# Performance work log

Hardware: AMD Instinct MI355X
Metric: run time of the kernel (lower is better)

The kernel has to match this reference:

```python
import jax, jax.numpy as jnp
import numpy as np

IN_CH = 2
K = 5
STRIDE = 1
NQ = IN_CH * K          # n_qubits = kernel_size * in_channels
DIM = 2 ** NQ           # quantum state dimension = 1024


def setup_inputs() -> dict:
    key = jax.random.key(0)
    k1, k2, k3 = jax.random.split(key, 3)
    x = jax.random.normal(k1, (16, IN_CH, 4096), dtype=jnp.float32)
    entangle_matrix = jax.random.normal(k2, (DIM, DIM), dtype=jnp.float32) / np.sqrt(DIM).astype(np.float32)
    theta = jax.random.uniform(k3, (NQ,), dtype=jnp.float32, minval=0.0, maxval=2.0 * np.pi)
    return {"x": x, "entangle_matrix": entangle_matrix, "theta": theta}


def _im2col(x):
    # torch: unfold(-1,K,stride) -> (B,C,nW,K); cat over channel dim along -1 -> (B,nW,C*K)
    B, C, L = x.shape
    nW = (L - K) // STRIDE + 1
    idx = jnp.arange(nW)[:, None] * STRIDE + jnp.arange(K)[None, :]   # (nW, K)
    cols = x[:, :, idx]                                               # (B, C, nW, K)
    cols = jnp.transpose(cols, (0, 2, 1, 3)).reshape(B * nW, C * K)   # channel-major last dim
    return cols, nW


def reference(x, entangle_matrix, theta):
    cols, nW = _im2col(x)           # (N, NQ) rotation angles, one per qubit
    N = cols.shape[0]
    # --- RY(x_i) angle encoding from |0...0>: product state of [cos(x/2), sin(x/2)] ---
    half = 0.5 * cols
    c, s = jnp.cos(half), jnp.sin(half)          # (N, NQ)
    state = jnp.ones((N, 1), dtype=x.dtype)
    for i in range(NQ):                          # loop over fixed small n_qubits
        qi = jnp.stack([c[:, i], s[:, i]], axis=-1)            # (N, 2)
        state = (state[:, :, None] * qi[:, None, :]).reshape(N, -1)
    # --- entangling layer: psi' = E @ psi (the custom kernel matmul) ---
    state = state @ entangle_matrix.T            # (N, DIM)
    # --- trainable per-qubit RY(theta_i) layer ---
    ct, st = jnp.cos(0.5 * theta), jnp.sin(0.5 * theta)
    for i in range(NQ):
        s4 = state.reshape(N, 2 ** i, 2, 2 ** (NQ - 1 - i))
        a0, a1 = s4[:, :, 0], s4[:, :, 1]
        state = jnp.stack([ct[i] * a0 - st[i] * a1,
                           st[i] * a0 + ct[i] * a1], axis=2).reshape(N, DIM)
    # --- measure <Z> on qubit 0 (most significant bit) ---
    p = (state * state).reshape(N, 2, DIM // 2)
    z = p[:, 0].sum(-1) - p[:, 1].sum(-1)        # (N,)
    B = x.shape[0]
    return z.reshape(B, 1, -1, nW)
```

## Files before the change

kernel.cpp:

```cpp
#include <hip/hip_runtime.h>
#include <math.h>

#define B_SZ   16
#define L_SZ   4096
#define NWIN   4092
#define U3     243
#define UPAD   256

#define APK_OFF 0
#define M_OFF   65536
#define EXTRA_OFF (M_OFF + 1048576)

typedef __attribute__((ext_vector_type(8))) __bf16 bf16x8;
typedef __attribute__((ext_vector_type(4))) float f32x4;

__device__ __forceinline__ float sel3(int t, float c, float s) {
    return t == 0 ? 1.0f : (t == 1 ? c : s);
}

__device__ __forceinline__ int apk_idx(int u, int v) {
    return (((u >> 4) * 8 + (v >> 5)) * 64 + ((u & 15) | (((v >> 3) & 3) << 4))) * 8 + (v & 7);
}

__device__ __forceinline__ void bfsplit(float x, float& hf, float& lf) {
    hf = __uint_as_float(__float_as_uint(x) & 0xFFFF0000u);
    lf = x - hf;
}

__global__ __launch_bounds__(256, 4) void mgemm_ker(const float* __restrict__ E,
                                                    const float* __restrict__ theta,
                                                    float* __restrict__ M,
                                                    float* __restrict__ Mp_extra) {
    __shared__ float SA[32][72];
    __shared__ float SB[32][72];
    __shared__ uint4 AfH[4 * 64], AfL[4 * 64];
    __shared__ uint4 BfH[4 * 64], BfL[4 * 64];

    int t = blockIdx.x;
    int bj = 0;
    while (t >= 16 - bj) { t -= 16 - bj; ++bj; }
    int bk = bj + t;
    int ks = blockIdx.z;
    int tid = threadIdx.x;
    int lane = tid & 63;
    int wave = tid >> 6;

    float th = theta[0];
    float st, ct;
    __sincosf(th, &st, &ct);

    f32x4 acc[4];
    #pragma unroll
    for (int kt = 0; kt < 4; ++kt) acc[kt] = (f32x4){0.f, 0.f, 0.f, 0.f};

    int kchunk = 1024 / gridDim.z;
    int k0 = ks * kchunk;
    int lr = tid >> 3;
    int lcq = (tid & 7) * 8;

    for (int d0 = k0; d0 < k0 + kchunk; d0 += 32) {
        bool hi = d0 >= 512;
        int dp = hi ? (d0 - 512) : (d0 + 512);
        float4 a0 = *(const float4*)&E[(d0 + lr) * 1024 + bj * 64 + lcq];
        float4 a1 = *(const float4*)&E[(d0 + lr) * 1024 + bj * 64 + lcq + 4];
        float4 q0 = *(const float4*)&E[(d0 + lr) * 1024 + bk * 64 + lcq];
        float4 q1 = *(const float4*)&E[(d0 + lr) * 1024 + bk * 64 + lcq + 4];
        float4 p0 = *(const float4*)&E[(dp + lr) * 1024 + bk * 64 + lcq];
        float4 p1 = *(const float4*)&E[(dp + lr) * 1024 + bk * 64 + lcq + 4];
        float4 y0, y1;
        if (!hi) {
            y0.x = ct * q0.x - st * p0.x; y0.y = ct * q0.y - st * p0.y;
            y0.z = ct * q0.z - st * p0.z; y0.w = ct * q0.w - st * p0.w;
            y1.x = ct * q1.x - st * p1.x; y1.y = ct * q1.y - st * p1.y;
            y1.z = ct * q1.z - st * p1.z; y1.w = ct * q1.w - st * p1.w;
        } else {
            y0.x = -st * p0.x - ct * q0.x; y0.y = -st * p0.y - ct * q0.y;
            y0.z = -st * p0.z - ct * q0.z; y0.w = -st * p0.w - ct * q0.w;
            y1.x = -st * p1.x - ct * q1.x; y1.y = -st * p1.y - ct * q1.y;
            y1.z = -st * p1.z - ct * q1.z; y1.w = -st * p1.w - ct * q1.w;
        }
        __syncthreads();
        *(float4*)&SA[lr][lcq] = a0;
        *(float4*)&SA[lr][lcq + 4] = a1;
        *(float4*)&SB[lr][lcq] = y0;
        *(float4*)&SB[lr][lcq + 4] = y1;
        __syncthreads();

        {
            unsigned ahw[4], alw[4], bhw[4], blw[4];
            float pah, pal, pbh, pbl;
            #pragma unroll
            for (int i = 0; i < 8; ++i) {
                float av = SA[wave * 8 + i][lane];
                float bv = SB[wave * 8 + i][lane];
                float ah, al, bh, bl;
                bfsplit(av, ah, al);
                bfsplit(bv, bh, bl);
                if (i & 1) {
                    ahw[i >> 1] = __byte_perm(__float_as_uint(pah), __float_as_uint(ah), 0x7632);
                    alw[i >> 1] = __byte_perm(__float_as_uint(pal), __float_as_uint(al), 0x7632);
                    bhw[i >> 1] = __byte_perm(__float_as_uint(pbh), __float_as_uint(bh), 0x7632);
                    blw[i >> 1] = __byte_perm(__float_as_uint(pbl), __float_as_uint(bl), 0x7632);
                } else { pah = ah; pal = al; pbh = bh; pbl = bl; }
            }
            int slot = ((lane >> 4) << 6) + (lane & 15) + (wave << 4);
            AfH[slot] = make_uint4(ahw[0], ahw[1], ahw[2], ahw[3]);
            AfL[slot] = make_uint4(alw[0], alw[1], alw[2], alw[3]);
            BfH[slot] = make_uint4(bhw[0], bhw[1], bhw[2], bhw[3]);
            BfL[slot] = make_uint4(blw[0], blw[1], blw[2], blw[3]);
        }
        __syncthreads();

        uint4 ahu = AfH[wave * 64 + lane];
        uint4 alu = AfL[wave * 64 + lane];
        bf16x8 ah = __builtin_bit_cast(bf16x8, ahu);
        bf16x8 al = __builtin_bit_cast(bf16x8, alu);
        #pragma unroll
        for (int kt = 0; kt < 4; ++kt) {
            uint4 bhu = BfH[kt * 64 + lane];
            uint4 blu = BfL[kt * 64 + lane];
            bf16x8 bh = __builtin_bit_cast(bf16x8, bhu);
            bf16x8 bl = __builtin_bit_cast(bf16x8, blu);
            acc[kt] = __builtin_amdgcn_mfma_f32_16x16x32_bf16(ah, bh, acc[kt], 0, 0, 0);
            acc[kt] = __builtin_amdgcn_mfma_f32_16x16x32_bf16(ah, bl, acc[kt], 0, 0, 0);
            acc[kt] = __builtin_amdgcn_mfma_f32_16x16x32_bf16(al, bh, acc[kt], 0, 0, 0);
        }
    }

    float* dst = (ks == 0) ? M : (Mp_extra + (ks - 1) * 1048576);
    #pragma unroll
    for (int kt = 0; kt < 4; ++kt) {
        #pragma unroll
        for (int i = 0; i < 4; ++i) {
            int r = bj * 64 + wave * 16 + ((lane >> 4) << 2) + i;
            int c = bk * 64 + kt * 16 + (lane & 15);
            dst[((r >> 5) * 32 + (c >> 5)) * 1024 + (r & 31) * 32 + (c & 31)] = acc[kt][i];
        }
    }
}

__global__ __launch_bounds__(256) void sum_ker(float* __restrict__ M,
                                               const float* __restrict__ Mp_extra,
                                               int S) {
    int i = blockIdx.x * 256 + threadIdx.x;
    float4 v = ((const float4*)M)[i];
    for (int s = 1; s < S; ++s) {
        float4 p = ((const float4*)(Mp_extra + (s - 1) * 1048576))[i];
        v.x += p.x; v.y += p.y; v.z += p.z; v.w += p.w;
    }
    ((float4*)M)[i] = v;
}

__global__ __launch_bounds__(256) void cwht_ker(const float* __restrict__ M,
                                                unsigned short* __restrict__ ApkH) {
    __shared__ float D[1024];
    int mx = blockIdx.x;
    int mxh = mx >> 5, mxl = mx & 31;
    int tid = threadIdx.x;
    float v[4];
    #pragma unroll
    for (int k = 0; k < 4; ++k) {
        int j = tid + k * 256;
        int jh = j >> 5, jl = j & 31;
        int kh = jh ^ mxh, kl = jl ^ mxl;
        int off;
        if ((jh >> 1) <= (kh >> 1)) off = ((jh * 32 + kh) * 32 + jl) * 32 + kl;
        else                        off = ((kh * 32 + jh) * 32 + kl) * 32 + jl;
        v[k] = M[off];
    }
    #pragma unroll
    for (int s = 0; s < 6; ++s) {
        int bit = (tid >> s) & 1;
        #pragma unroll
        for (int k = 0; k < 4; ++k) {
            float p = __shfl_xor(v[k], 1 << s, 64);
            v[k] = bit ? (p - v[k]) : (v[k] + p);
        }
    }
    #pragma unroll
    for (int k = 0; k < 4; ++k) D[tid + k * 256] = v[k];
    __syncthreads();
    {
        int b6 = (tid >> 6) & 1, b7 = (tid >> 7) & 1;
        #pragma unroll
        for (int k = 0; k < 4; ++k) {
            float p64  = D[(tid ^ 64)  + k * 256];
            float p128 = D[(tid ^ 128) + k * 256];
            float p192 = D[(tid ^ 192) + k * 256];
            float ta = b6 ? (p64 - v[k])   : (v[k] + p64);
            float tb = b6 ? (p192 - p128)  : (p128 + p192);
            v[k] = b7 ? (tb - ta) : (ta + tb);
        }
    }
    {
        float a0 = v[0] + v[1], a1 = v[0] - v[1], a2 = v[2] + v[3], a3 = v[2] - v[3];
        v[0] = a0 + a2; v[1] = a1 + a3; v[2] = a0 - a2; v[3] = a1 - a3;
    }
    #pragma unroll
    for (int k = 0; k < 4; ++k) {
        int mz = tid + k * 256;
        if (mz & mx) continue;
        int u = 0, vv = 0;
        #pragma unroll
        for (int i = 0; i < 5; ++i) {
            int bit = 9 - i;
            int tt = ((mx >> bit) & 1) ? 2 : (((mz >> bit) & 1) ? 1 : 0);
            u = u * 3 + tt;
        }
        #pragma unroll
        for (int i = 5; i < 10; ++i) {
            int bit = 9 - i;
            int tt = ((mx >> bit) & 1) ? 2 : (((mz >> bit) & 1) ? 1 : 0);
            vv = vv * 3 + tt;
        }
        float val = v[k] * (1.0f / 1024.0f);
        unsigned hh = __float_as_uint(val) & 0xFFFF0000u;
        float lf = val - __uint_as_float(hh);
        unsigned ll = __float_as_uint(lf) >> 16;
        int idx = apk_idx(u, vv);
        ApkH[idx] = (unsigned short)(hh >> 16);
        ApkH[idx + 65536] = (unsigned short)ll;
    }
    if (mx == 0) {
        for (int e = tid; e < 13 * 256; e += 256) {
            int u = 243 + (e >> 8), vv = e & 255;
            int idx = apk_idx(u, vv);
            ApkH[idx] = 0; ApkH[idx + 65536] = 0;
        }
        for (int e = tid; e < 243 * 13; e += 256) {
            int u = e / 13, vv = 243 + (e - (e / 13) * 13);
            int idx = apk_idx(u, vv);
            ApkH[idx] = 0; ApkH[idx + 65536] = 0;
        }
    }
}

__global__ __launch_bounds__(256, 3) void main_ker(const float* __restrict__ x,
                                                   const uint4* __restrict__ Apk,
                                                   float* __restrict__ out) {
    __shared__ float trg[4][68];
    __shared__ __align__(16) unsigned char arena[49408];
    uint4* Abuf = (uint4*)arena;
    unsigned short* F1h = (unsigned short*)(arena + 32768);
    float* F0 = (float*)arena;
    __shared__ float red[16][16];

    int tid = threadIdx.x;
    int w0 = blockIdx.x * 64;
    int b  = blockIdx.y;
    int lane = tid & 63;
    int wave = tid >> 6;
    int wb = tid & 63;
    int wu = __builtin_amdgcn_readfirstlane(wave);

    for (int p = tid; p < 68; p += 256) {
        int pos = w0 + p;
        bool ok = pos < L_SZ;
        float x1 = ok ? x[b * 8192 + 4096 + pos] : 0.f;
        float x0 = ok ? x[b * 8192 + pos] : 0.f;
        float c1v, s1v, c0v, s0v;
        __sincosf(x1, &s1v, &c1v);
        __sincosf(x0, &s0v, &c0v);
        if (!ok) { c1v = 0.f; s1v = 0.f; c0v = 0.f; s0v = 0.f; }
        trg[0][p] = c1v; trg[1][p] = s1v; trg[2][p] = c0v; trg[3][p] = s0v;
    }

    f32x4 acc[4][4];
    #pragma unroll
    for (int ut = 0; ut < 4; ++ut)
        #pragma unroll
        for (int wt = 0; wt < 4; ++wt)
            acc[ut][wt] = (f32x4){0.f, 0.f, 0.f, 0.f};

    __syncthreads();

    float c1r[5], s1r[5];
    #pragma unroll
    for (int k = 0; k < 5; ++k) { c1r[k] = trg[0][wb + k]; s1r[k] = trg[1][wb + k]; }

    #pragma unroll 1
    for (int h = 0; h < 2; ++h) {
        if (h) __syncthreads();
        {
            int gv = h * 128 + wu * 32;
            int t0 = gv / 81; int rr = gv - t0 * 81;
            int t1 = rr / 27; rr -= t1 * 27;
            int t2 = rr / 9;  rr -= t2 * 9;
            int t3 = rr / 3;  int t4 = rr - t3 * 3;
            float g0 = sel3(t0, c1r[0], s1r[0]);
            float g1 = sel3(t1, c1r[1], s1r[1]);
            float g2 = sel3(t2, c1r[2], s1r[2]);
            float g3 = sel3(t3, c1r[3], s1r[3]);
            float p0123 = g0 * g1 * g2 * g3;
            #pragma unroll
            for (int p8 = 0; p8 < 4; ++p8) {
                unsigned hw[4];
                unsigned prevr;
                #pragma unroll
                for (int i = 0; i < 8; ++i) {
                    float val = p0123 * sel3(t4, c1r[4], s1r[4]);
                    unsigned rb = (__float_as_uint(val) + 0x8000u) >> 16;
                    if (i & 1) hw[i >> 1] = prevr | (rb << 16);
                    else       prevr = rb;
                    if (++t4 == 3) { t4 = 0;
                        if (++t3 == 3) { t3 = 0;
                            if (++t2 == 3) { t2 = 0;
                                if (++t1 == 3) { t1 = 0; ++t0; g0 = sel3(t0, c1r[0], s1r[0]); }
                                g1 = sel3(t1, c1r[1], s1r[1]);
                            }
                            g2 = sel3(t2, c1r[2], s1r[2]);
                        }
                        g3 = sel3(t3, c1r[3], s1r[3]);
                        p0123 = g0 * g1 * g2 * g3;
                    }
                }
                int vp = wu * 4 + p8;
                *(uint4*)&F1h[(vp * 65 + wb) * 8] = make_uint4(hw[0], hw[1], hw[2], hw[3]);
            }
        }
        __syncthreads();

        #pragma unroll
        for (int kl = 0; kl < 4; ++kl) {
            int ks = h * 4 + kl;
            #pragma unroll
            for (int ut = 0; ut < 4; ++ut) {
                #pragma unroll
                for (int pl = 0; pl < 2; ++pl) {
                    int gidx = pl * 8192 + ((wave * 4 + ut) * 8 + ks) * 64 + lane;
                    int slot = (wave * 4 + ut) * 2 + pl;
                    __builtin_amdgcn_global_load_lds(
                        (const __attribute__((address_space(1))) unsigned int*)(Apk + gidx),
                        (__attribute__((address_space(3))) unsigned int*)(Abuf + slot * 64 + lane),
                        16, 0, 0);
                }
            }
            asm volatile("s_waitcnt vmcnt(0)" ::: "memory");
            __builtin_amdgcn_sched_barrier(0);
            int vp = kl * 4 + (lane >> 4);
            #pragma unroll
            for (int wt = 0; wt < 4; ++wt) {
                int off = (vp * 65 + wt * 16 + (lane & 15)) * 8;
                uint4 b_u = *(const uint4*)&F1h[off];
                bf16x8 bb = __builtin_bit_cast(bf16x8, b_u);
                #pragma unroll
                for (int ut = 0; ut < 4; ++ut) {
                    uint4 ahu = Abuf[((wave * 4 + ut) * 2 + 0) * 64 + lane];
                    uint4 alu = Abuf[((wave * 4 + ut) * 2 + 1) * 64 + lane];
                    bf16x8 ah = __builtin_bit_cast(bf16x8, ahu);
                    bf16x8 al = __builtin_bit_cast(bf16x8, alu);
                    acc[ut][wt] = __builtin_amdgcn_mfma_f32_16x16x32_bf16(ah, bb, acc[ut][wt], 0, 0, 0);
                    acc[ut][wt] = __builtin_amdgcn_mfma_f32_16x16x32_bf16(al, bb, acc[ut][wt], 0, 0, 0);
                }
            }
        }
    }

    int c = lane & 15;
    float c0b[5], s0b[5];
    #pragma unroll
    for (int k = 0; k < 5; ++k) { c0b[k] = trg[2][wb + k]; s0b[k] = trg[3][wb + k]; }
    float zcol[4] = {0.f, 0.f, 0.f, 0.f};

    __syncthreads();
    #pragma unroll 1
    for (int hp = 0; hp < 2; ++hp) {
        if (hp) __syncthreads();
        {
            int gu = hp * 128 + wu * 32;
            int t0 = gu / 81; int rr = gu - t0 * 81;
            int t1 = rr / 27; rr -= t1 * 27;
            int t2 = rr / 9;  rr -= t2 * 9;
            int t3 = rr / 3;  int t4 = rr - t3 * 3;
            float g0 = sel3(t0, c0b[0], s0b[0]);
            float g1 = sel3(t1, c0b[1], s0b[1]);
            float g2 = sel3(t2, c0b[2], s0b[2]);
            float g3 = sel3(t3, c0b[3], s0b[3]);
            float p0123 = g0 * g1 * g2 * g3;
            #pragma unroll
            for (int s = 0; s < 32; ++s) {
                float val = p0123 * sel3(t4, c0b[4], s0b[4]);
                F0[(wu * 32 + s) * 65 + wb] = val;
                if (++t4 == 3) { t4 = 0;
                    if (++t3 == 3) { t3 = 0;
                        if (++t2 == 3) { t2 = 0;
                            if (++t1 == 3) { t1 = 0; ++t0; g0 = sel3(t0, c0b[0], s0b[0]); }
                            g1 = sel3(t1, c0b[1], s0b[1]);
                        }
                        g2 = sel3(t2, c0b[2], s0b[2]);
                    }
                    g3 = sel3(t3, c0b[3], s0b[3]);
                    p0123 = g0 * g1 * g2 * g3;
                }
            }
        }
        __syncthreads();
        if ((wave >> 1) == hp) {
            int wloc = wave & 1;
            int qb = (lane >> 4) << 2;
            #pragma unroll
            for (int ut = 0; ut < 4; ++ut) {
                #pragma unroll
                for (int r = 0; r < 4; ++r) {
                    int uloc = wloc * 64 + ut * 16 + qb + r;
                    #pragma unroll
                    for (int wt = 0; wt < 4; ++wt)
                        zcol[wt] += F0[uloc * 65 + wt * 16 + c] * acc[ut][wt][r];
                }
            }
        }
    }

    #pragma unroll
    for (int wt = 0; wt < 4; ++wt) {
        float v = zcol[wt];
        v += __shfl_xor(v, 16, 64);
        v += __shfl_xor(v, 32, 64);
        if ((lane >> 4) == 0) red[wave * 4 + wt][lane] = v;
    }
    __syncthreads();
    if (tid < 64) {
        int wt = tid >> 4, cc = tid & 15;
        float z = red[0 * 4 + wt][cc] + red[1 * 4 + wt][cc]
                + red[2 * 4 + wt][cc] + red[3 * 4 + wt][cc];
        int w = wt * 16 + cc;
        if (w0 + w < NWIN) out[b * NWIN + w0 + w] = z;
    }
}

extern "C" void kernel_launch(void* const* d_in, const int* in_sizes, int n_in,
                              void* d_out, int out_size, void* d_ws, size_t ws_size,
                              hipStream_t stream) {
    const float* x     = (const float*)d_in[0];
    const float* E     = (const float*)d_in[1];
    const float* theta = (const float*)d_in[2];
    float* out = (float*)d_out;
    float* ws = (float*)d_ws;

    uint4* Apk = (uint4*)(ws + APK_OFF);
    float* M   = ws + M_OFF;
    float* Mx  = ws + EXTRA_OFF;

    size_t need4 = (size_t)(EXTRA_OFF + 3 * 1048576) * 4;
    size_t need2 = (size_t)(EXTRA_OFF + 1 * 1048576) * 4;
    int S = (ws_size >= need4) ? 4 : ((ws_size >= need2) ? 2 : 1);

    mgemm_ker<<<dim3(136, 1, S), 256, 0, stream>>>(E, theta, M, Mx);
    if (S > 1) sum_ker<<<1024, 256, 0, stream>>>(M, Mx, S);
    cwht_ker<<<1024, 256, 0, stream>>>(M, (unsigned short*)Apk);
    main_ker<<<dim3(64, 16), 256, 0, stream>>>(x, Apk, out);
}
```

Baseline: 64.81 us.

## Fuse split-K sum into cwht, cut split to 2, prefetch A tiles

The separate sum kernel is removed and its partial-sum accumulation now happens inside cwht_ker's gather load. The mgemm split-K factor drops from 4 to 2. In main_ker, A tiles are first copied from LDS into registers, then the next k-step's global-to-LDS loads are issued before the MFMAs run, so the load latency overlaps with compute. The trade-offs are more register pressure and less parallelism in mgemm.

```diff
diff --git a/kernel.cpp b/kernel.cpp
--- a/kernel.cpp
+++ b/kernel.cpp
@@ -139,19 +139,9 @@
     }
 }
 
-__global__ __launch_bounds__(256) void sum_ker(float* __restrict__ M,
-                                               const float* __restrict__ Mp_extra,
-                                               int S) {
-    int i = blockIdx.x * 256 + threadIdx.x;
-    float4 v = ((const float4*)M)[i];
-    for (int s = 1; s < S; ++s) {
-        float4 p = ((const float4*)(Mp_extra + (s - 1) * 1048576))[i];
-        v.x += p.x; v.y += p.y; v.z += p.z; v.w += p.w;
-    }
-    ((float4*)M)[i] = v;
-}
-
 __global__ __launch_bounds__(256) void cwht_ker(const float* __restrict__ M,
+                                                const float* __restrict__ Mp_extra,
+                                                int S,
                                                 unsigned short* __restrict__ ApkH) {
     __shared__ float D[1024];
     int mx = blockIdx.x;
@@ -166,7 +156,9 @@
         int off;
         if ((jh >> 1) <= (kh >> 1)) off = ((jh * 32 + kh) * 32 + jl) * 32 + kl;
         else                        off = ((kh * 32 + jh) * 32 + kl) * 32 + jl;
-        v[k] = M[off];
+        float t = M[off];
+        for (int s = 1; s < S; ++s) t += Mp_extra[(s - 1) * 1048576 + off];
+        v[k] = t;
     }
     #pragma unroll
     for (int s = 0; s < 6; ++s) {
@@ -252,6 +244,19 @@
     int wave = tid >> 6;
     int wb = tid & 63;
     int wu = __builtin_amdgcn_readfirstlane(wave);
+
+    #pragma unroll
+    for (int ut = 0; ut < 4; ++ut) {
+        #pragma unroll
+        for (int pl = 0; pl < 2; ++pl) {
+            int gidx = pl * 8192 + ((wave * 4 + ut) * 8 + 0) * 64 + lane;
+            int slot = (wave * 4 + ut) * 2 + pl;
+            __builtin_amdgcn_global_load_lds(
+                (const __attribute__((address_space(1))) unsigned int*)(Apk + gidx),
+                (__attribute__((address_space(3))) unsigned int*)(Abuf + slot * 64 + lane),
+                16, 0, 0);
+        }
+    }
 
     for (int p = tid; p < 68; p += 256) {
         int pos = w0 + p;
@@ -323,20 +328,30 @@
         #pragma unroll
         for (int kl = 0; kl < 4; ++kl) {
             int ks = h * 4 + kl;
-            #pragma unroll
-            for (int ut = 0; ut < 4; ++ut) {
-                #pragma unroll
-                for (int pl = 0; pl < 2; ++pl) {
-                    int gidx = pl * 8192 + ((wave * 4 + ut) * 8 + ks) * 64 + lane;
-                    int slot = (wave * 4 + ut) * 2 + pl;
-                    __builtin_amdgcn_global_load_lds(
-                        (const __attribute__((address_space(1))) unsigned int*)(Apk + gidx),
-                        (__attribute__((address_space(3))) unsigned int*)(Abuf + slot * 64 + lane),
-                        16, 0, 0);
-                }
-            }
             asm volatile("s_waitcnt vmcnt(0)" ::: "memory");
             __builtin_amdgcn_sched_barrier(0);
+            uint4 a_h[4], a_l[4];
+            #pragma unroll
+            for (int ut = 0; ut < 4; ++ut) {
+                a_h[ut] = Abuf[((wave * 4 + ut) * 2 + 0) * 64 + lane];
+                a_l[ut] = Abuf[((wave * 4 + ut) * 2 + 1) * 64 + lane];
+            }
+            asm volatile("s_waitcnt lgkmcnt(0)" ::: "memory");
+            __builtin_amdgcn_sched_barrier(0);
+            if (ks < 7) {
+                #pragma unroll
+                for (int ut = 0; ut < 4; ++ut) {
+                    #pragma unroll
+                    for (int pl = 0; pl < 2; ++pl) {
+                        int gidx = pl * 8192 + ((wave * 4 + ut) * 8 + ks + 1) * 64 + lane;
+                        int slot = (wave * 4 + ut) * 2 + pl;
+                        __builtin_amdgcn_global_load_lds(
+                            (const __attribute__((address_space(1))) unsigned int*)(Apk + gidx),
+                            (__attribute__((address_space(3))) unsigned int*)(Abuf + slot * 64 + lane),
+                            16, 0, 0);
+                    }
+                }
+            }
             int vp = kl * 4 + (lane >> 4);
             #pragma unroll
             for (int wt = 0; wt < 4; ++wt) {
@@ -345,10 +360,8 @@
                 bf16x8 bb = __builtin_bit_cast(bf16x8, b_u);
                 #pragma unroll
                 for (int ut = 0; ut < 4; ++ut) {
-                    uint4 ahu = Abuf[((wave * 4 + ut) * 2 + 0) * 64 + lane];
-                    uint4 alu = Abuf[((wave * 4 + ut) * 2 + 1) * 64 + lane];
-                    bf16x8 ah = __builtin_bit_cast(bf16x8, ahu);
-                    bf16x8 al = __builtin_bit_cast(bf16x8, alu);
+                    bf16x8 ah = __builtin_bit_cast(bf16x8, a_h[ut]);
+                    bf16x8 al = __builtin_bit_cast(bf16x8, a_l[ut]);
                     acc[ut][wt] = __builtin_amdgcn_mfma_f32_16x16x32_bf16(ah, bb, acc[ut][wt], 0, 0, 0);
                     acc[ut][wt] = __builtin_amdgcn_mfma_f32_16x16x32_bf16(al, bb, acc[ut][wt], 0, 0, 0);
                 }
@@ -441,12 +454,10 @@
     float* M   = ws + M_OFF;
     float* Mx  = ws + EXTRA_OFF;
 
-    size_t need4 = (size_t)(EXTRA_OFF + 3 * 1048576) * 4;
     size_t need2 = (size_t)(EXTRA_OFF + 1 * 1048576) * 4;
-    int S = (ws_size >= need4) ? 4 : ((ws_size >= need2) ? 2 : 1);
+    int S = (ws_size >= need2) ? 2 : 1;
 
     mgemm_ker<<<dim3(136, 1, S), 256, 0, stream>>>(E, theta, M, Mx);
-    if (S > 1) sum_ker<<<1024, 256, 0, stream>>>(M, Mx, S);
-    cwht_ker<<<1024, 256, 0, stream>>>(M, (unsigned short*)Apk);
+    cwht_ker<<<1024, 256, 0, stream>>>(M, Mx, S, (unsigned short*)Apk);
     main_ker<<<dim3(64, 16), 256, 0, stream>>>(x, Apk, out);
 }
```

Result: slower. 80.95 us (+24.9%).
